# Kernel optimization log

Measured on AMD Instinct MI355X. Metric: run time of the kernel, lower is better.

Reference implementation:

```python
import jax, jax.numpy as jnp
import numpy as np

N_NODES = 50000
N_EDGES = 600000
IN_C = 128
HID = 128
OUT_C = 32
N_GRAPHS = 64


def setup_inputs() -> dict:
    key = jax.random.key(0)
    ks = jax.random.split(key, 12)
    x = jax.random.normal(ks[0], (N_NODES, IN_C), dtype=jnp.float32)
    edge_index = jax.random.randint(ks[1], (2, N_EDGES), 0, N_NODES, dtype=jnp.int64)
    batch = jnp.sort(jax.random.randint(ks[2], (N_NODES,), 0, N_GRAPHS, dtype=jnp.int64))
    s1 = 1.0 / np.sqrt(IN_C)
    s2 = 1.0 / np.sqrt(HID)
    # SAGEConv: out = lin_l(mean_neighbors) + lin_r(x); lin_l has bias, lin_r has none
    W1l = jax.random.uniform(ks[3], (HID, IN_C), minval=-s1, maxval=s1, dtype=jnp.float32)
    b1 = jax.random.uniform(ks[4], (HID,), minval=-s1, maxval=s1, dtype=jnp.float32)
    W1r = jax.random.uniform(ks[5], (HID, IN_C), minval=-s1, maxval=s1, dtype=jnp.float32)
    W2l = jax.random.uniform(ks[6], (HID, HID), minval=-s2, maxval=s2, dtype=jnp.float32)
    b2 = jax.random.uniform(ks[7], (HID,), minval=-s2, maxval=s2, dtype=jnp.float32)
    W2r = jax.random.uniform(ks[8], (HID, HID), minval=-s2, maxval=s2, dtype=jnp.float32)
    Wlin = jax.random.uniform(ks[9], (OUT_C, HID), minval=-s2, maxval=s2, dtype=jnp.float32)
    blin = jax.random.uniform(ks[10], (OUT_C,), minval=-s2, maxval=s2, dtype=jnp.float32)
    return {"x": x, "edge_index": edge_index, "batch": batch,
            "W1l": W1l, "b1": b1, "W1r": W1r,
            "W2l": W2l, "b2": b2, "W2r": W2r,
            "Wlin": Wlin, "blin": blin}


def _sage_conv(x, src, dst, Wl, bl, Wr):
    # mean aggregation of source-node features onto destination nodes
    msg_sum = jax.ops.segment_sum(x[src], dst, num_segments=N_NODES)  # [N, d]
    deg = jax.ops.segment_sum(jnp.ones((src.shape[0],), x.dtype), dst, num_segments=N_NODES)
    mean = msg_sum / jnp.maximum(deg, 1.0)[:, None]
    return mean @ Wl.T + bl + x @ Wr.T


def reference(x, edge_index, batch, W1l, b1, W1r, W2l, b2, W2r, Wlin, blin):
    src, dst = edge_index[0], edge_index[1]
    h = jax.nn.relu(_sage_conv(x, src, dst, W1l, b1, W1r))
    h = jax.nn.relu(_sage_conv(h, src, dst, W2l, b2, W2r))
    # global mean pool over graph ids
    gsum = jax.ops.segment_sum(h, batch, num_segments=N_GRAPHS)        # [G, HID]
    cnt = jax.ops.segment_sum(jnp.ones((h.shape[0],), h.dtype), batch, num_segments=N_GRAPHS)
    pooled = gsum / jnp.maximum(cnt, 1.0)[:, None]
    return pooled @ Wlin.T + blin
```

## Files before the change

### kernel.cpp

```cpp
#include <hip/hip_runtime.h>
#include <hip/hip_fp16.h>

#define N_NODES 50000
#define N_EDGES 600000
#define N_GRAPHS 64
#define HID 128
#define OUT_C 32

#define SCAN_BLK 256
#define N_SCAN_BLOCKS ((N_NODES + SCAN_BLK - 1) / SCAN_BLK)

typedef __attribute__((ext_vector_type(8))) _Float16 half8;
typedef __attribute__((ext_vector_type(4))) _Float16 half4;
typedef __attribute__((ext_vector_type(4))) float f32x4;

__global__ __launch_bounds__(256) void prep_kernel(
    const float* __restrict__ x,
    const float* __restrict__ W1l, const float* __restrict__ W1r,
    const float* __restrict__ W2l, const float* __restrict__ W2r,
    __half* __restrict__ xh, __half* __restrict__ Wt1, __half* __restrict__ Wt2) {
    int b = blockIdx.x;
    if (b < 16) {
        int idx = b * 256 + threadIdx.x;
        for (int i = idx; i < 65536; i += 4096) {
            int which = i >> 15;
            int j = i & 32767;
            int n = j >> 8, k = j & 255;
            const float* Wl = which ? W2l : W1l;
            const float* Wr = which ? W2r : W1r;
            float a = (k < 128) ? Wl[n * 128 + k] : Wr[n * 128 + (k - 128)];
            (which ? Wt2 : Wt1)[j] = __float2half(a);
        }
    } else {
        int i = ((b - 16) * 256 + threadIdx.x) * 4;
        if (i < N_NODES * 128) {
            float4 v = *(const float4*)(x + i);
            __half2 a = __floats2half2_rn(v.x, v.y);
            __half2 b2 = __floats2half2_rn(v.z, v.w);
            uint2 st;
            st.x = *(const unsigned int*)&a;
            st.y = *(const unsigned int*)&b2;
            *(uint2*)(xh + i) = st;
        }
    }
}

__global__ void deg_kernel(const int* __restrict__ dst, int* __restrict__ deg, int E) {
    int e = blockIdx.x * 256 + threadIdx.x;
    if (e < E) atomicAdd(&deg[dst[e]], 1);
}

__global__ __launch_bounds__(SCAN_BLK) void scan_blocksum(
    const int* __restrict__ deg, int* __restrict__ bsum) {
    __shared__ int s[SCAN_BLK];
    int i = blockIdx.x * SCAN_BLK + threadIdx.x;
    s[threadIdx.x] = (i < N_NODES) ? deg[i] : 0;
    __syncthreads();
    for (int off = SCAN_BLK / 2; off > 0; off >>= 1) {
        if (threadIdx.x < off) s[threadIdx.x] += s[threadIdx.x + off];
        __syncthreads();
    }
    if (threadIdx.x == 0) bsum[blockIdx.x] = s[0];
}

__global__ __launch_bounds__(256) void scan_boff(
    const int* __restrict__ bsum, int* __restrict__ boff, int* __restrict__ rowptr) {
    __shared__ int s[256];
    int t = threadIdx.x;
    int v = (t < N_SCAN_BLOCKS) ? bsum[t] : 0;
    s[t] = v;
    __syncthreads();
    for (int off = 1; off < 256; off <<= 1) {
        int u = (t >= off) ? s[t - off] : 0;
        __syncthreads();
        s[t] += u;
        __syncthreads();
    }
    if (t < N_SCAN_BLOCKS) boff[t] = s[t] - v;
    if (t == N_SCAN_BLOCKS - 1) rowptr[N_NODES] = s[t];
}

__global__ __launch_bounds__(SCAN_BLK) void scan_emit(
    const int* __restrict__ deg, const int* __restrict__ boff,
    int* __restrict__ rowptr, float* __restrict__ invdeg) {
    __shared__ int s[SCAN_BLK];
    int i = blockIdx.x * SCAN_BLK + threadIdx.x;
    int t = threadIdx.x;
    int v = (i < N_NODES) ? deg[i] : 0;
    s[t] = v;
    __syncthreads();
    for (int off = 1; off < SCAN_BLK; off <<= 1) {
        int u = (t >= off) ? s[t - off] : 0;
        __syncthreads();
        s[t] += u;
        __syncthreads();
    }
    if (i < N_NODES) {
        rowptr[i] = boff[blockIdx.x] + s[t] - v;
        invdeg[i] = 1.0f / fmaxf((float)v, 1.0f);
    }
}

__global__ void fill_kernel(const int* __restrict__ src, const int* __restrict__ dst,
                            const int* __restrict__ rowptr, int* __restrict__ cursor,
                            int* __restrict__ eidx, int E) {
    int e = blockIdx.x * 256 + threadIdx.x;
    if (e < E) {
        int d = dst[e];
        int pos = atomicAdd(&cursor[d], 1);
        eidx[rowptr[d] + pos] = src[e];
    }
}

#define AGG_ACC(vv, aa) { aa.x += (float)vv[0]; aa.y += (float)vv[1]; \
                          aa.z += (float)vv[2]; aa.w += (float)vv[3]; }

__global__ __launch_bounds__(256) void aggregate_f16(
    const __half* __restrict__ feat16, const int* __restrict__ rowptr,
    const int* __restrict__ eidx, const float* __restrict__ invdeg,
    __half* __restrict__ mean16) {
    const int wave = threadIdx.x >> 6;
    const int lane = threadIdx.x & 63;
    const int nh   = lane >> 5;
    const int sub  = lane & 31;
    const int node = blockIdx.x * 8 + wave * 2 + nh;
    const bool act = (node < N_NODES);
    int beg = 0, end = 0;
    if (act) { beg = rowptr[node]; end = rowptr[node + 1]; }
    const size_t coff = (size_t)sub * 4;

    float4 a0 = {0.f,0.f,0.f,0.f}, a1 = {0.f,0.f,0.f,0.f};
    float4 a2 = {0.f,0.f,0.f,0.f}, a3 = {0.f,0.f,0.f,0.f};
    int i = beg;
    for (; i + 8 <= end; i += 8) {
        int s0 = eidx[i+0], s1 = eidx[i+1], s2 = eidx[i+2], s3 = eidx[i+3];
        int s4 = eidx[i+4], s5 = eidx[i+5], s6 = eidx[i+6], s7 = eidx[i+7];
        half4 v0 = *(const half4*)(feat16 + (size_t)s0 * 128 + coff);
        half4 v1 = *(const half4*)(feat16 + (size_t)s1 * 128 + coff);
        half4 v2 = *(const half4*)(feat16 + (size_t)s2 * 128 + coff);
        half4 v3 = *(const half4*)(feat16 + (size_t)s3 * 128 + coff);
        half4 v4 = *(const half4*)(feat16 + (size_t)s4 * 128 + coff);
        half4 v5 = *(const half4*)(feat16 + (size_t)s5 * 128 + coff);
        half4 v6 = *(const half4*)(feat16 + (size_t)s6 * 128 + coff);
        half4 v7 = *(const half4*)(feat16 + (size_t)s7 * 128 + coff);
        AGG_ACC(v0, a0); AGG_ACC(v1, a1); AGG_ACC(v2, a2); AGG_ACC(v3, a3);
        AGG_ACC(v4, a0); AGG_ACC(v5, a1); AGG_ACC(v6, a2); AGG_ACC(v7, a3);
    }
    if (i + 4 <= end) {
        int s0 = eidx[i+0], s1 = eidx[i+1], s2 = eidx[i+2], s3 = eidx[i+3];
        half4 v0 = *(const half4*)(feat16 + (size_t)s0 * 128 + coff);
        half4 v1 = *(const half4*)(feat16 + (size_t)s1 * 128 + coff);
        half4 v2 = *(const half4*)(feat16 + (size_t)s2 * 128 + coff);
        half4 v3 = *(const half4*)(feat16 + (size_t)s3 * 128 + coff);
        AGG_ACC(v0, a0); AGG_ACC(v1, a1); AGG_ACC(v2, a2); AGG_ACC(v3, a3);
        i += 4;
    }
    if (i + 2 <= end) {
        int s0 = eidx[i+0], s1 = eidx[i+1];
        half4 v0 = *(const half4*)(feat16 + (size_t)s0 * 128 + coff);
        half4 v1 = *(const half4*)(feat16 + (size_t)s1 * 128 + coff);
        AGG_ACC(v0, a0); AGG_ACC(v1, a1);
        i += 2;
    }
    if (i < end) {
        int s0 = eidx[i];
        half4 v0 = *(const half4*)(feat16 + (size_t)s0 * 128 + coff);
        AGG_ACC(v0, a0);
    }

    if (act) {
        const float sc = invdeg[node];
        half4 r;
        r[0] = (_Float16)(((a0.x + a1.x) + (a2.x + a3.x)) * sc);
        r[1] = (_Float16)(((a0.y + a1.y) + (a2.y + a3.y)) * sc);
        r[2] = (_Float16)(((a0.z + a1.z) + (a2.z + a3.z)) * sc);
        r[3] = (_Float16)(((a0.w + a1.w) + (a2.w + a3.w)) * sc);
        *(half4*)(mean16 + (size_t)node * 128 + coff) = r;
    }
}

#define GBM 64
#define BPAD 8

__global__ __launch_bounds__(256) void sage_gemm_f16(
    const __half* __restrict__ mean16, const __half* __restrict__ feat16,
    const __half* __restrict__ Wt, const float* __restrict__ bias,
    __half* __restrict__ out16, int M) {
    __shared__ __align__(16) __half Bs[128][256 + BPAD];

    const int tid = threadIdx.x;
    const int wave = tid >> 6;
    const int lane = tid & 63;
    const int l15 = lane & 15;
    const int quad = lane >> 4;
    const int row0 = blockIdx.x * GBM;
    const int gi_a = min(row0 + wave * 16 + l15, M - 1);

    for (int id = tid; id < 128 * 32; id += 256) {
        int n = id >> 5;
        int kc = (id & 31) * 8;
        *(half8*)&Bs[n][kc] = *(const half8*)(Wt + (size_t)n * 256 + kc);
    }

    half8 af[8];
#pragma unroll
    for (int kb = 0; kb < 8; ++kb) {
        const int k0 = kb * 32;
        const __half* ap = (k0 < 128)
            ? (mean16 + (size_t)gi_a * 128 + k0 + quad * 8)
            : (feat16 + (size_t)gi_a * 128 + (k0 - 128) + quad * 8);
        af[kb] = *(const half8*)ap;
    }

    f32x4 acc[8];
#pragma unroll
    for (int t = 0; t < 8; ++t) acc[t] = (f32x4){0.f, 0.f, 0.f, 0.f};

    __syncthreads();

#pragma unroll
    for (int kb = 0; kb < 8; ++kb) {
#pragma unroll
        for (int t = 0; t < 8; ++t) {
            const half8 b = *(const half8*)&Bs[t * 16 + l15][kb * 32 + quad * 8];
            acc[t] = __builtin_amdgcn_mfma_f32_16x16x32_f16(af[kb], b, acc[t], 0, 0, 0);
        }
    }

#pragma unroll
    for (int r = 0; r < 4; ++r) {
        int gi = row0 + wave * 16 + quad * 4 + r;
        if (gi < M) {
#pragma unroll
            for (int t = 0; t < 8; ++t) {
                int col = t * 16 + l15;
                float v = fmaxf(acc[t][r] + bias[col], 0.f);
                out16[(size_t)gi * 128 + col] = __float2half(v);
            }
        }
    }
}

#define POOL_PARTS 4
__global__ __launch_bounds__(256) void pool_graph(
    const __half* __restrict__ h, const int* __restrict__ batch,
    float* __restrict__ pooled, int* __restrict__ gcnt) {
    const int g = blockIdx.x >> 2;
    const int part = blockIdx.x & 3;
    int lo = 0, hi = N_NODES;
    while (lo < hi) { int mid = (lo + hi) >> 1; if (batch[mid] < g) lo = mid + 1; else hi = mid; }
    const int start = lo;
    hi = N_NODES;
    while (lo < hi) { int mid = (lo + hi) >> 1; if (batch[mid] < g + 1) lo = mid + 1; else hi = mid; }
    const int end = lo;

    const int t = threadIdx.x;
    if (part == 0 && t == 0) gcnt[g] = end - start;

    const int c4 = (t & 31) * 4;
    const int rg = t >> 5;
    float4 acc = {0.f, 0.f, 0.f, 0.f};
    for (int n = start + part * 8 + rg; n < end; n += 8 * POOL_PARTS) {
        const __half2* p = (const __half2*)(h + (size_t)n * 128 + c4);
        float2 f0 = __half22float2(p[0]);
        float2 f1 = __half22float2(p[1]);
        acc.x += f0.x; acc.y += f0.y; acc.z += f1.x; acc.w += f1.y;
    }
    __shared__ float sm[8][132];
    sm[rg][c4 + 0] = acc.x;
    sm[rg][c4 + 1] = acc.y;
    sm[rg][c4 + 2] = acc.z;
    sm[rg][c4 + 3] = acc.w;
    __syncthreads();
    if (t < 128) {
        float s = 0.f;
#pragma unroll
        for (int r = 0; r < 8; ++r) s += sm[r][t];
        atomicAdd(&pooled[g * 128 + t], s);
    }
}

__global__ void final_kernel(const float* __restrict__ pooled, const int* __restrict__ gcnt,
                             const float* __restrict__ Wlin, const float* __restrict__ blin,
                             float* __restrict__ out) {
    int g = blockIdx.x;
    int j = threadIdx.x;
    float inv = 1.0f / fmaxf((float)gcnt[g], 1.0f);
    float sum = blin[j];
    const float* prow = pooled + g * 128;
    const float* wrow = Wlin + j * 128;
    for (int c = 0; c < 128; ++c) sum += prow[c] * inv * wrow[c];
    out[g * 32 + j] = sum;
}

extern "C" void kernel_launch(void* const* d_in, const int* in_sizes, int n_in,
                              void* d_out, int out_size, void* d_ws, size_t ws_size,
                              hipStream_t stream) {
    const float* x    = (const float*)d_in[0];
    const int*   src  = (const int*)d_in[1];
    const int*   dst  = ((const int*)d_in[1]) + N_EDGES;
    const int*   batch= (const int*)d_in[2];
    const float* W1l  = (const float*)d_in[3];
    const float* b1   = (const float*)d_in[4];
    const float* W1r  = (const float*)d_in[5];
    const float* W2l  = (const float*)d_in[6];
    const float* b2   = (const float*)d_in[7];
    const float* W2r  = (const float*)d_in[8];
    const float* Wlin = (const float*)d_in[9];
    const float* blin = (const float*)d_in[10];
    float* out = (float*)d_out;

    __half* xh     = (__half*)d_ws;
    __half* mean16 = xh + 6400000;
    __half* h1_16  = mean16 + 6400000;
    __half* h2_16  = h1_16 + 6400000;
    __half* Wt1    = h2_16 + 6400000;
    __half* Wt2    = Wt1 + 32768;
    float* pooled  = (float*)(Wt2 + 32768);
    int*   gcnt    = (int*)(pooled + N_GRAPHS * 128);
    float* invdeg  = (float*)(gcnt + 64);
    int*   degi    = (int*)(invdeg + N_NODES);
    int*   cursor  = degi + N_NODES;
    int*   rowptr  = cursor + N_NODES;
    int*   eidx    = rowptr + N_NODES + 1;
    int*   bsum    = eidx + N_EDGES;
    int*   boff    = bsum + N_SCAN_BLOCKS;

    hipMemsetAsync(degi, 0, (size_t)(2 * N_NODES) * sizeof(int), stream);
    hipMemsetAsync(pooled, 0, (size_t)(N_GRAPHS * 128) * sizeof(float), stream);

    prep_kernel<<<16 + (N_NODES * 128 / 4 + 255) / 256, 256, 0, stream>>>(
        x, W1l, W1r, W2l, W2r, xh, Wt1, Wt2);

    deg_kernel<<<(N_EDGES + 255) / 256, 256, 0, stream>>>(dst, degi, N_EDGES);
    scan_blocksum<<<N_SCAN_BLOCKS, SCAN_BLK, 0, stream>>>(degi, bsum);
    scan_boff<<<1, 256, 0, stream>>>(bsum, boff, rowptr);
    scan_emit<<<N_SCAN_BLOCKS, SCAN_BLK, 0, stream>>>(degi, boff, rowptr, invdeg);
    fill_kernel<<<(N_EDGES + 255) / 256, 256, 0, stream>>>(src, dst, rowptr, cursor, eidx, N_EDGES);

    const int gemm_grid = (N_NODES + GBM - 1) / GBM;
    const int agg_grid = (N_NODES + 7) / 8;

    aggregate_f16<<<agg_grid, 256, 0, stream>>>(xh, rowptr, eidx, invdeg, mean16);
    sage_gemm_f16<<<gemm_grid, 256, 0, stream>>>(mean16, xh, Wt1, b1, h1_16, N_NODES);

    aggregate_f16<<<agg_grid, 256, 0, stream>>>(h1_16, rowptr, eidx, invdeg, mean16);
    sage_gemm_f16<<<gemm_grid, 256, 0, stream>>>(mean16, h1_16, Wt2, b2, h2_16, N_NODES);

    pool_graph<<<N_GRAPHS * POOL_PARTS, 256, 0, stream>>>(h2_16, batch, pooled, gcnt);
    final_kernel<<<N_GRAPHS, 32, 0, stream>>>(pooled, gcnt, Wlin, blin, out);
}
```

Baseline: 263.8 us.

## Fuse CSR build and prep into cooperative kernel; fuse pooling with final linear

Replaces the two memsets, prep, degree, three scan and fill kernels with one cooperative kernel of 512 blocks that uses grid-wide syncs between phases. Pooling now writes per-part partial sums, and the last block to finish (found with an atomic counter) computes the final linear layer, which removes the atomics on pooled and one more launch. This cuts launch count and inter-kernel gaps. The cost is five grid barriers and lower parallelism in the grid-stride conversion loops and in the single-block final matmul.

```diff
diff --git a/kernel.cpp b/kernel.cpp
--- a/kernel.cpp
+++ b/kernel.cpp
@@ -1,5 +1,8 @@
 #include <hip/hip_runtime.h>
 #include <hip/hip_fp16.h>
+#include <hip/hip_cooperative_groups.h>
+
+namespace cg = cooperative_groups;
 
 #define N_NODES 50000
 #define N_EDGES 600000
@@ -7,67 +10,58 @@
 #define HID 128
 #define OUT_C 32
 
-#define SCAN_BLK 256
-#define N_SCAN_BLOCKS ((N_NODES + SCAN_BLK - 1) / SCAN_BLK)
+#define COOP_BLOCKS 512
 
 typedef __attribute__((ext_vector_type(8))) _Float16 half8;
 typedef __attribute__((ext_vector_type(4))) _Float16 half4;
 typedef __attribute__((ext_vector_type(4))) float f32x4;
 
-__global__ __launch_bounds__(256) void prep_kernel(
+__global__ __launch_bounds__(256, 2) void coop_prep_csr(
     const float* __restrict__ x,
     const float* __restrict__ W1l, const float* __restrict__ W1r,
     const float* __restrict__ W2l, const float* __restrict__ W2r,
-    __half* __restrict__ xh, __half* __restrict__ Wt1, __half* __restrict__ Wt2) {
-    int b = blockIdx.x;
-    if (b < 16) {
-        int idx = b * 256 + threadIdx.x;
-        for (int i = idx; i < 65536; i += 4096) {
-            int which = i >> 15;
-            int j = i & 32767;
-            int n = j >> 8, k = j & 255;
-            const float* Wl = which ? W2l : W1l;
-            const float* Wr = which ? W2r : W1r;
-            float a = (k < 128) ? Wl[n * 128 + k] : Wr[n * 128 + (k - 128)];
-            (which ? Wt2 : Wt1)[j] = __float2half(a);
-        }
-    } else {
-        int i = ((b - 16) * 256 + threadIdx.x) * 4;
-        if (i < N_NODES * 128) {
-            float4 v = *(const float4*)(x + i);
-            __half2 a = __floats2half2_rn(v.x, v.y);
-            __half2 b2 = __floats2half2_rn(v.z, v.w);
-            uint2 st;
-            st.x = *(const unsigned int*)&a;
-            st.y = *(const unsigned int*)&b2;
-            *(uint2*)(xh + i) = st;
-        }
-    }
-}
-
-__global__ void deg_kernel(const int* __restrict__ dst, int* __restrict__ deg, int E) {
-    int e = blockIdx.x * 256 + threadIdx.x;
-    if (e < E) atomicAdd(&deg[dst[e]], 1);
-}
-
-__global__ __launch_bounds__(SCAN_BLK) void scan_blocksum(
-    const int* __restrict__ deg, int* __restrict__ bsum) {
-    __shared__ int s[SCAN_BLK];
-    int i = blockIdx.x * SCAN_BLK + threadIdx.x;
-    s[threadIdx.x] = (i < N_NODES) ? deg[i] : 0;
-    __syncthreads();
-    for (int off = SCAN_BLK / 2; off > 0; off >>= 1) {
-        if (threadIdx.x < off) s[threadIdx.x] += s[threadIdx.x + off];
-        __syncthreads();
-    }
-    if (threadIdx.x == 0) bsum[blockIdx.x] = s[0];
-}
-
-__global__ __launch_bounds__(256) void scan_boff(
-    const int* __restrict__ bsum, int* __restrict__ boff, int* __restrict__ rowptr) {
+    const int* __restrict__ src, const int* __restrict__ dst,
+    __half* __restrict__ xh, __half* __restrict__ Wt1, __half* __restrict__ Wt2,
+    int* __restrict__ degi, int* __restrict__ cursor, int* __restrict__ rowptr,
+    int* __restrict__ eidx, float* __restrict__ invdeg,
+    int* __restrict__ bsum, int* __restrict__ boff, int* __restrict__ done) {
+    cg::grid_group grid = cg::this_grid();
+    const int t = threadIdx.x;
+    const int b = blockIdx.x;
+    const int gtid = b * 256 + t;
+    const int gstride = COOP_BLOCKS * 256;
     __shared__ int s[256];
-    int t = threadIdx.x;
-    int v = (t < N_SCAN_BLOCKS) ? bsum[t] : 0;
+
+    for (int i = gtid; i < N_NODES; i += gstride) { degi[i] = 0; cursor[i] = 0; }
+    if (gtid == 0) *done = 0;
+    for (int i = gtid; i < 65536; i += gstride) {
+        int which = i >> 15;
+        int j = i & 32767;
+        int n = j >> 8, k = j & 255;
+        const float* Wl = which ? W2l : W1l;
+        const float* Wr = which ? W2r : W1r;
+        float a = (k < 128) ? Wl[n * 128 + k] : Wr[n * 128 + (k - 128)];
+        (which ? Wt2 : Wt1)[j] = __float2half(a);
+    }
+    for (int i = gtid * 4; i < N_NODES * 128; i += gstride * 4) {
+        float4 v = *(const float4*)(x + i);
+        __half2 a = __floats2half2_rn(v.x, v.y);
+        __half2 c = __floats2half2_rn(v.z, v.w);
+        uint2 st;
+        st.x = *(const unsigned int*)&a;
+        st.y = *(const unsigned int*)&c;
+        *(uint2*)(xh + i) = st;
+    }
+    grid.sync();
+
+    for (int e = gtid; e < N_EDGES; e += gstride) atomicAdd(&degi[dst[e]], 1);
+    grid.sync();
+
+    const int npb = (N_NODES + COOP_BLOCKS - 1) / COOP_BLOCKS;
+    const int base = b * npb;
+    const int idx = base + t;
+    int v = 0;
+    if (t < npb && idx < N_NODES) v = degi[idx];
     s[t] = v;
     __syncthreads();
     for (int off = 1; off < 256; off <<= 1) {
@@ -76,36 +70,38 @@
         s[t] += u;
         __syncthreads();
     }
-    if (t < N_SCAN_BLOCKS) boff[t] = s[t] - v;
-    if (t == N_SCAN_BLOCKS - 1) rowptr[N_NODES] = s[t];
-}
-
-__global__ __launch_bounds__(SCAN_BLK) void scan_emit(
-    const int* __restrict__ deg, const int* __restrict__ boff,
-    int* __restrict__ rowptr, float* __restrict__ invdeg) {
-    __shared__ int s[SCAN_BLK];
-    int i = blockIdx.x * SCAN_BLK + threadIdx.x;
-    int t = threadIdx.x;
-    int v = (i < N_NODES) ? deg[i] : 0;
-    s[t] = v;
-    __syncthreads();
-    for (int off = 1; off < SCAN_BLK; off <<= 1) {
-        int u = (t >= off) ? s[t - off] : 0;
+    int incl = s[t];
+    if (t == 255) bsum[b] = incl;
+    if (t < npb && idx < N_NODES) rowptr[idx] = incl - v;
+    grid.sync();
+
+    if (b == 0) {
+        int v0 = bsum[2 * t], v1 = bsum[2 * t + 1];
+        s[t] = v0 + v1;
         __syncthreads();
-        s[t] += u;
-        __syncthreads();
-    }
-    if (i < N_NODES) {
-        rowptr[i] = boff[blockIdx.x] + s[t] - v;
-        invdeg[i] = 1.0f / fmaxf((float)v, 1.0f);
-    }
-}
-
-__global__ void fill_kernel(const int* __restrict__ src, const int* __restrict__ dst,
-                            const int* __restrict__ rowptr, int* __restrict__ cursor,
-                            int* __restrict__ eidx, int E) {
-    int e = blockIdx.x * 256 + threadIdx.x;
-    if (e < E) {
+        for (int off = 1; off < 256; off <<= 1) {
+            int u = (t >= off) ? s[t - off] : 0;
+            __syncthreads();
+            s[t] += u;
+            __syncthreads();
+        }
+        int excl = s[t] - (v0 + v1);
+        boff[2 * t] = excl;
+        boff[2 * t + 1] = excl + v0;
+        if (t == 255) rowptr[N_NODES] = s[t];
+    }
+    grid.sync();
+
+    {
+        int bo = boff[b];
+        if (t < npb && idx < N_NODES) {
+            rowptr[idx] += bo;
+            invdeg[idx] = 1.0f / fmaxf((float)v, 1.0f);
+        }
+    }
+    grid.sync();
+
+    for (int e = gtid; e < N_EDGES; e += gstride) {
         int d = dst[e];
         int pos = atomicAdd(&cursor[d], 1);
         eidx[rowptr[d] + pos] = src[e];
@@ -242,9 +238,11 @@
 }
 
 #define POOL_PARTS 4
-__global__ __launch_bounds__(256) void pool_graph(
+__global__ __launch_bounds__(256) void pool_final(
     const __half* __restrict__ h, const int* __restrict__ batch,
-    float* __restrict__ pooled, int* __restrict__ gcnt) {
+    const float* __restrict__ Wlin, const float* __restrict__ blin,
+    float* __restrict__ pooled_parts, int* __restrict__ gcnt,
+    int* __restrict__ done, float* __restrict__ out) {
     const int g = blockIdx.x >> 2;
     const int part = blockIdx.x & 3;
     int lo = 0, hi = N_NODES;
@@ -276,21 +274,35 @@
         float s = 0.f;
 #pragma unroll
         for (int r = 0; r < 8; ++r) s += sm[r][t];
-        atomicAdd(&pooled[g * 128 + t], s);
-    }
-}
-
-__global__ void final_kernel(const float* __restrict__ pooled, const int* __restrict__ gcnt,
-                             const float* __restrict__ Wlin, const float* __restrict__ blin,
-                             float* __restrict__ out) {
-    int g = blockIdx.x;
-    int j = threadIdx.x;
-    float inv = 1.0f / fmaxf((float)gcnt[g], 1.0f);
-    float sum = blin[j];
-    const float* prow = pooled + g * 128;
-    const float* wrow = Wlin + j * 128;
-    for (int c = 0; c < 128; ++c) sum += prow[c] * inv * wrow[c];
-    out[g * 32 + j] = sum;
+        pooled_parts[(size_t)blockIdx.x * 128 + t] = s;
+    }
+
+    __threadfence();
+    __shared__ int lastflag;
+    if (t == 0) {
+        int old = atomicAdd(done, 1);
+        lastflag = (old == (int)gridDim.x - 1);
+    }
+    __syncthreads();
+    if (!lastflag) return;
+    __threadfence();
+
+    for (int task = t; task < N_GRAPHS * OUT_C; task += 256) {
+        int gg = task >> 5;
+        int j = task & 31;
+        float inv = 1.0f / fmaxf((float)gcnt[gg], 1.0f);
+        float sum = blin[j];
+        const float* w = Wlin + j * 128;
+        const float* p0 = pooled_parts + (size_t)(gg * 4 + 0) * 128;
+        const float* p1 = pooled_parts + (size_t)(gg * 4 + 1) * 128;
+        const float* p2 = pooled_parts + (size_t)(gg * 4 + 2) * 128;
+        const float* p3 = pooled_parts + (size_t)(gg * 4 + 3) * 128;
+        for (int c = 0; c < 128; ++c) {
+            float p = (p0[c] + p1[c]) + (p2[c] + p3[c]);
+            sum += p * inv * w[c];
+        }
+        out[task] = sum;
+    }
 }
 
 extern "C" void kernel_launch(void* const* d_in, const int* in_sizes, int n_in,
@@ -316,27 +328,26 @@
     __half* h2_16  = h1_16 + 6400000;
     __half* Wt1    = h2_16 + 6400000;
     __half* Wt2    = Wt1 + 32768;
-    float* pooled  = (float*)(Wt2 + 32768);
-    int*   gcnt    = (int*)(pooled + N_GRAPHS * 128);
-    float* invdeg  = (float*)(gcnt + 64);
-    int*   degi    = (int*)(invdeg + N_NODES);
+    float* pooled_parts = (float*)(Wt2 + 32768);
+    float* invdeg  = pooled_parts + 32768;
+    int*   gcnt    = (int*)(invdeg + N_NODES);
+    int*   done    = gcnt + 64;
+    int*   degi    = done + 1;
     int*   cursor  = degi + N_NODES;
     int*   rowptr  = cursor + N_NODES;
     int*   eidx    = rowptr + N_NODES + 1;
     int*   bsum    = eidx + N_EDGES;
-    int*   boff    = bsum + N_SCAN_BLOCKS;
-
-    hipMemsetAsync(degi, 0, (size_t)(2 * N_NODES) * sizeof(int), stream);
-    hipMemsetAsync(pooled, 0, (size_t)(N_GRAPHS * 128) * sizeof(float), stream);
-
-    prep_kernel<<<16 + (N_NODES * 128 / 4 + 255) / 256, 256, 0, stream>>>(
-        x, W1l, W1r, W2l, W2r, xh, Wt1, Wt2);
-
-    deg_kernel<<<(N_EDGES + 255) / 256, 256, 0, stream>>>(dst, degi, N_EDGES);
-    scan_blocksum<<<N_SCAN_BLOCKS, SCAN_BLK, 0, stream>>>(degi, bsum);
-    scan_boff<<<1, 256, 0, stream>>>(bsum, boff, rowptr);
-    scan_emit<<<N_SCAN_BLOCKS, SCAN_BLK, 0, stream>>>(degi, boff, rowptr, invdeg);
-    fill_kernel<<<(N_EDGES + 255) / 256, 256, 0, stream>>>(src, dst, rowptr, cursor, eidx, N_EDGES);
+    int*   boff    = bsum + COOP_BLOCKS;
+
+    void* cargs[] = {
+        (void*)&x, (void*)&W1l, (void*)&W1r, (void*)&W2l, (void*)&W2r,
+        (void*)&src, (void*)&dst,
+        (void*)&xh, (void*)&Wt1, (void*)&Wt2,
+        (void*)&degi, (void*)&cursor, (void*)&rowptr, (void*)&eidx,
+        (void*)&invdeg, (void*)&bsum, (void*)&boff, (void*)&done
+    };
+    hipLaunchCooperativeKernel((void*)coop_prep_csr, dim3(COOP_BLOCKS), dim3(256),
+                               cargs, 0, stream);
 
     const int gemm_grid = (N_NODES + GBM - 1) / GBM;
     const int agg_grid = (N_NODES + 7) / 8;
@@ -347,6 +358,6 @@
     aggregate_f16<<<agg_grid, 256, 0, stream>>>(h1_16, rowptr, eidx, invdeg, mean16);
     sage_gemm_f16<<<gemm_grid, 256, 0, stream>>>(mean16, h1_16, Wt2, b2, h2_16, N_NODES);
 
-    pool_graph<<<N_GRAPHS * POOL_PARTS, 256, 0, stream>>>(h2_16, batch, pooled, gcnt);
-    final_kernel<<<N_GRAPHS, 32, 0, stream>>>(pooled, gcnt, Wlin, blin, out);
-}
+    pool_final<<<N_GRAPHS * POOL_PARTS, 256, 0, stream>>>(
+        h2_16, batch, Wlin, blin, pooled_parts, gcnt, done, out);
+}
```

Result: slower. 632.4 us (+139.7%).
